# Performance work log

Measured on AMD Instinct MI355X. Metric: run time of the kernel, lower is better.

The kernel has to match this reference:

```python
import jax, jax.numpy as jnp
import numpy as np

NUM_BUCKETS = 2000003
HASH_DIM = 64
MODEL_DIM = 1024
HASH_MULT = 92821


def setup_inputs() -> dict:
    key = jax.random.key(0)
    k_ids, k_tab = jax.random.split(key, 2)
    input_ids = jax.random.randint(k_ids, (4, 8192), 0, 50257, dtype=jnp.int64)
    # learned params: embedding table (std=0.01 init), projection (zero-init flag in source)
    table = 0.01 * jax.random.normal(k_tab, (NUM_BUCKETS, HASH_DIM), dtype=jnp.float32)
    proj_w = jnp.zeros((MODEL_DIM, HASH_DIM), dtype=jnp.float32)  # nn.Linear stores [out, in]
    return {"input_ids": input_ids, "table": table, "proj_w": proj_w}


def reference(input_ids, table, proj_w):
    # prev token ids: shift right with a leading zero per batch row
    prev_ids = jnp.concatenate(
        [jnp.zeros((input_ids.shape[0], 1), dtype=input_ids.dtype), input_ids[:, :-1]],
        axis=1,
    )
    h = (prev_ids * HASH_MULT + input_ids) % NUM_BUCKETS  # [B, S] bucket ids
    emb = table[h]  # [B, S, hash_dim] gather
    # CastedLinear: F.linear(x, w.to(x.dtype)) -> x @ w.T
    return jnp.einsum("bsh,mh->bsm", emb, proj_w.astype(emb.dtype))
```

## Files before the change

### kernel.cpp

```cpp
#include <hip/hip_runtime.h>

#define NUM_BUCKETS 2000003
#define HASH_MULT   92821
#define SEQ         8192
#define NTOK        32768
#define MDIM        1024
#define HDIM        64
#define TT          64

__global__ __launch_bounds__(256) void hash_kernel(const int* __restrict__ ids,
                                                   int* __restrict__ hbuf) {
    int t = blockIdx.x * 256 + threadIdx.x;
    if (t >= NTOK) return;
    unsigned long long cur  = (unsigned long long)(unsigned int)ids[t];
    unsigned long long prev = ((t & (SEQ - 1)) == 0)
                                  ? 0ull
                                  : (unsigned long long)(unsigned int)ids[t - 1];
    hbuf[t] = (int)((prev * (unsigned long long)HASH_MULT + cur) %
                    (unsigned long long)NUM_BUCKETS);
}

__global__ __launch_bounds__(256) void bigram_kernel(const int*   __restrict__ hbuf,
                                                     const float* __restrict__ table,
                                                     const float* __restrict__ W,
                                                     float*       __restrict__ out) {
    const int lane = threadIdx.x & 63;
    const int wid  = threadIdx.x >> 6;
    const int m    = blockIdx.y * 256 + wid * 64 + lane;

    float4 w[16];
    const float4* Wv = (const float4*)(W + (size_t)m * HDIM);
#pragma unroll
    for (int i = 0; i < 16; ++i) w[i] = Wv[i];

    const int t0 = blockIdx.x * TT;
    for (int tt = 0; tt < TT; ++tt) {
        const int t = t0 + tt;
        const int h = __builtin_amdgcn_readfirstlane(hbuf[t]);
        const float4* e = (const float4*)(table + (size_t)h * HDIM);

        float4 acc = {0.f, 0.f, 0.f, 0.f};
#pragma unroll
        for (int k = 0; k < 16; ++k) {
            float4 ev = e[k];
            acc.x = fmaf(w[k].x, ev.x, acc.x);
            acc.y = fmaf(w[k].y, ev.y, acc.y);
            acc.z = fmaf(w[k].z, ev.z, acc.z);
            acc.w = fmaf(w[k].w, ev.w, acc.w);
        }
        out[(size_t)t * MDIM + m] = (acc.x + acc.y) + (acc.z + acc.w);
    }
}

extern "C" void kernel_launch(void* const* d_in, const int* in_sizes, int n_in,
                              void* d_out, int out_size, void* d_ws, size_t ws_size,
                              hipStream_t stream) {
    const int*   ids   = (const int*)d_in[0];
    const float* table = (const float*)d_in[1];
    const float* W     = (const float*)d_in[2];
    float*       out   = (float*)d_out;
    int*         hbuf  = (int*)d_ws;

    hash_kernel<<<NTOK / 256, 256, 0, stream>>>(ids, hbuf);

    dim3 grid(NTOK / TT, MDIM / 256);
    bigram_kernel<<<grid, 256, 0, stream>>>(hbuf, table, W, out);
}
```

Before: 675.9 us.

## Stage gathered embedding rows in LDS and cover full model dim per block

Each block now runs 1024 threads covering all output columns for 64 tokens. The 64 gathered table rows are loaded cooperatively into shared memory once per block, so the four column-blocks no longer each re-gather the same rows from global memory. The embedding reads then come from LDS broadcasts instead of scalar-uniform global loads. The cost is larger blocks with a 64-float4 register load of W per thread, which limits occupancy, and a barrier before compute.

```diff
diff --git a/kernel.cpp b/kernel.cpp
--- a/kernel.cpp
+++ b/kernel.cpp
@@ -1,12 +1,12 @@
 #include <hip/hip_runtime.h>
 
-#define NUM_BUCKETS 2000003
-#define HASH_MULT   92821
+#define NUM_BUCKETS 2000003ull
+#define HASH_MULT   92821ull
 #define SEQ         8192
 #define NTOK        32768
 #define MDIM        1024
 #define HDIM        64
-#define TT          64
+#define G           64
 
 __global__ __launch_bounds__(256) void hash_kernel(const int* __restrict__ ids,
                                                    int* __restrict__ hbuf) {
@@ -16,29 +16,35 @@
     unsigned long long prev = ((t & (SEQ - 1)) == 0)
                                   ? 0ull
                                   : (unsigned long long)(unsigned int)ids[t - 1];
-    hbuf[t] = (int)((prev * (unsigned long long)HASH_MULT + cur) %
-                    (unsigned long long)NUM_BUCKETS);
+    hbuf[t] = (int)((prev * HASH_MULT + cur) % NUM_BUCKETS);
 }
 
-__global__ __launch_bounds__(256) void bigram_kernel(const int*   __restrict__ hbuf,
-                                                     const float* __restrict__ table,
-                                                     const float* __restrict__ W,
-                                                     float*       __restrict__ out) {
-    const int lane = threadIdx.x & 63;
-    const int wid  = threadIdx.x >> 6;
-    const int m    = blockIdx.y * 256 + wid * 64 + lane;
+__global__ __launch_bounds__(1024, 4) void bigram_kernel(const int*   __restrict__ hbuf,
+                                                         const float* __restrict__ table,
+                                                         const float* __restrict__ W,
+                                                         float*       __restrict__ out) {
+    __shared__ float rows[G * HDIM];
+
+    const int m = threadIdx.x;
+
+    {
+        const int r = m >> 4;
+        const int q = m & 15;
+        const int h = hbuf[blockIdx.x * G + r];
+        const float4 v = *(const float4*)(table + (size_t)h * HDIM + q * 4);
+        *(float4*)(&rows[r * HDIM + q * 4]) = v;
+    }
 
     float4 w[16];
     const float4* Wv = (const float4*)(W + (size_t)m * HDIM);
 #pragma unroll
     for (int i = 0; i < 16; ++i) w[i] = Wv[i];
 
-    const int t0 = blockIdx.x * TT;
-    for (int tt = 0; tt < TT; ++tt) {
-        const int t = t0 + tt;
-        const int h = __builtin_amdgcn_readfirstlane(hbuf[t]);
-        const float4* e = (const float4*)(table + (size_t)h * HDIM);
+    __syncthreads();
 
+    const size_t obase = (size_t)blockIdx.x * G * MDIM + m;
+    for (int t = 0; t < G; ++t) {
+        const float4* e = (const float4*)(&rows[t * HDIM]);
         float4 acc = {0.f, 0.f, 0.f, 0.f};
 #pragma unroll
         for (int k = 0; k < 16; ++k) {
@@ -48,7 +54,7 @@
             acc.z = fmaf(w[k].z, ev.z, acc.z);
             acc.w = fmaf(w[k].w, ev.w, acc.w);
         }
-        out[(size_t)t * MDIM + m] = (acc.x + acc.y) + (acc.z + acc.w);
+        out[obase + (size_t)t * MDIM] = (acc.x + acc.y) + (acc.z + acc.w);
     }
 }
 
@@ -62,7 +68,5 @@
     int*         hbuf  = (int*)d_ws;
 
     hash_kernel<<<NTOK / 256, 256, 0, stream>>>(ids, hbuf);
-
-    dim3 grid(NTOK / TT, MDIM / 256);
-    bigram_kernel<<<grid, 256, 0, stream>>>(hbuf, table, W, out);
+    bigram_kernel<<<NTOK / G, 1024, 0, stream>>>(hbuf, table, W, out);
 }
```

Result: slower. 1.039 ms (+53.8%).
